# Kernel optimization log

Measured on AMD Instinct MI355X. Metric: run time of the kernel, lower is better.

## Reference

```python
import math
import jax, jax.numpy as jnp
import numpy as np

N_HEAD = 12
HEAD_DIM = 64
NEG = -1e9

def setup_inputs() -> dict:
    key = jax.random.key(0)
    k1, k2, k3 = jax.random.split(key, 3)
    B, T, C = 16, 1024, 768
    x = jax.random.normal(k1, (B, T, C), dtype=jnp.float32)
    attention_mask = jnp.ones((B, T), dtype=jnp.int32)
    W_attn = jax.random.normal(k2, (C, 3 * C), dtype=jnp.float32) * 0.02
    b_attn = jnp.zeros((3 * C,), dtype=jnp.float32)
    W_proj = jax.random.normal(k3, (C, C), dtype=jnp.float32) * 0.02
    b_proj = jnp.zeros((C,), dtype=jnp.float32)
    return {"x": x, "attention_mask": attention_mask, "W_attn": W_attn,
            "b_attn": b_attn, "W_proj": W_proj, "b_proj": b_proj}

def reference(x, attention_mask, W_attn, b_attn, W_proj, b_proj):
    B, T, C = x.shape
    H, D = N_HEAD, HEAD_DIM
    qkv = x @ W_attn + b_attn                       # [B,T,3C]
    q, k, v = jnp.split(qkv, 3, axis=-1)
    q = q.reshape(B, T, H, D).transpose(0, 2, 1, 3)  # [B,H,T,D]
    k = k.reshape(B, T, H, D).transpose(0, 2, 1, 3)
    v = v.reshape(B, T, H, D).transpose(0, 2, 1, 3)
    att = jnp.einsum('bhqd,bhkd->bhqk', q, k) / math.sqrt(D)  # [B,H,T,T]
    causal = jnp.tril(jnp.ones((T, T), dtype=bool))[None, None]
    key_mask = (attention_mask[:, None, None, :] != 0)          # [B,1,1,T]
    # masked_fill(-inf) then replace inf with -1e9 == set masked to -1e9
    att = jnp.where(causal & key_mask, att, NEG)
    att = jax.nn.softmax(att, axis=-1)
    query_mask = attention_mask[:, None, :, None].astype(att.dtype)  # [B,1,T,1]
    att = att * query_mask
    y = jnp.einsum('bhqk,bhkd->bhqd', att, v)        # [B,H,T,D]
    y = y.transpose(0, 2, 1, 3).reshape(B, T, C)
    return y @ W_proj + b_proj
```

## Files before the change

### kernel.cpp

```cpp
#include <hip/hip_runtime.h>
#include <stdint.h>

typedef unsigned short u16;
typedef unsigned int u32;
typedef __attribute__((ext_vector_type(8))) short short8;
typedef __attribute__((ext_vector_type(4))) float f32x4;
typedef __attribute__((ext_vector_type(4))) unsigned short u16x4;

#define LDS_AS __attribute__((address_space(3)))
#define GLB_AS __attribute__((address_space(1)))

__device__ __forceinline__ u16 f2bf(float f) {
  u32 u = __float_as_uint(f);
  u = (u + 0x7FFFu + ((u >> 16) & 1u)) >> 16;
  return (u16)u;
}

__device__ __forceinline__ void gload_lds16(const u16* g, u16* l) {
  __builtin_amdgcn_global_load_lds((const GLB_AS u32*)g, (LDS_AS u32*)l, 16, 0, 0);
}

__device__ __forceinline__ f32x4 mfma16(short8 a, short8 b, f32x4 c) {
  return __builtin_amdgcn_mfma_f32_16x16x32_bf16(a, b, c, 0, 0, 0);
}

__global__ __launch_bounds__(256) void k_cvt(const float* __restrict__ in,
                                             u16* __restrict__ out, int n4) {
  int i = blockIdx.x * 256 + threadIdx.x;
  if (i >= n4) return;
  f32x4 v = ((const f32x4*)in)[i];
  u16x4 o = {f2bf(v[0]), f2bf(v[1]), f2bf(v[2]), f2bf(v[3])};
  ((u16x4*)out)[i] = o;
}

__global__ __launch_bounds__(256) void k_transpose_cvt(const float* __restrict__ W,
                                                       u16* __restrict__ Wt, int K, int N) {
  __shared__ float tile[32][33];
  int n0 = blockIdx.x * 32;
  int k0 = blockIdx.y * 32;
  int tx = threadIdx.x & 31, ty = threadIdx.x >> 5;
#pragma unroll
  for (int i = 0; i < 4; i++) {
    int k = k0 + ty + i * 8;
    tile[ty + i * 8][tx] = W[(size_t)k * N + n0 + tx];
  }
  __syncthreads();
#pragma unroll
  for (int i = 0; i < 4; i++) {
    int n = n0 + ty + i * 8;
    Wt[(size_t)n * K + k0 + tx] = f2bf(tile[tx][ty + i * 8]);
  }
}

template <int MODE>
__global__ __launch_bounds__(256) void k_gemm(const u16* __restrict__ A,
                                              const u16* __restrict__ Bt,
                                              const float* __restrict__ bias,
                                              void* __restrict__ C, u16* __restrict__ vTo,
                                              int M, int N, int K) {
  __shared__ __align__(16) u16 As[2][128 * 64];
  __shared__ __align__(16) u16 Bs[2][128 * 64];
  const int nwg = gridDim.x;
  const int wgo = blockIdx.x;
  const int cpx = nwg >> 3;
  const int swz = (wgo & 7) * cpx + (wgo >> 3);
  const int ntn = N >> 7;
  const int tm = swz / ntn, tn = swz % ntn;
  const int m0 = tm << 7, n0 = tn << 7;
  const int tid = threadIdx.x;
  const int lane = tid & 63, w = tid >> 6;
  const int wm = (w >> 1) << 6, wn = (w & 1) << 6;
  const int fr = lane & 15, kg = lane >> 4;

  f32x4 acc[4][4];
#pragma unroll
  for (int i = 0; i < 4; i++)
#pragma unroll
    for (int j = 0; j < 4; j++) acc[i][j] = (f32x4){0.f, 0.f, 0.f, 0.f};

  const int rs = tid >> 3;
  const int ck = (((tid & 7) ^ (rs & 7)) << 3);
  const u16* ga = A + (size_t)(m0 + rs) * K + ck;
  const u16* gb = Bt + (size_t)(n0 + rs) * K + ck;
  const size_t row32 = (size_t)32 * K;

#define GSTAGE(buf, kt)                                                      \
  {                                                                          \
    const int ko = (kt) * 64;                                                \
    _Pragma("unroll") for (int s = 0; s < 4; ++s) {                          \
      gload_lds16(ga + s * row32 + ko, &As[buf][s * 2048 + tid * 8]);        \
    }                                                                        \
    _Pragma("unroll") for (int s = 0; s < 4; ++s) {                          \
      gload_lds16(gb + s * row32 + ko, &Bs[buf][s * 2048 + tid * 8]);        \
    }                                                                        \
  }

  const int KT = K >> 6;
  GSTAGE(0, 0);

  for (int kt = 0; kt < KT; ++kt) {
    const int cur = kt & 1;
    if (kt + 1 < KT) {
      GSTAGE(cur ^ 1, kt + 1);
      asm volatile("s_waitcnt vmcnt(8)" ::: "memory");
    } else {
      asm volatile("s_waitcnt vmcnt(0)" ::: "memory");
    }
    __builtin_amdgcn_sched_barrier(0);
    __builtin_amdgcn_s_barrier();
    __builtin_amdgcn_sched_barrier(0);

#pragma unroll
    for (int kk = 0; kk < 2; ++kk) {
      short8 af[4], bf[4];
      const int cs = ((kk * 4 + kg) ^ (fr & 7)) << 3;
#pragma unroll
      for (int mi = 0; mi < 4; mi++)
        af[mi] = *(const short8*)&As[cur][(wm + mi * 16 + fr) * 64 + cs];
#pragma unroll
      for (int nj = 0; nj < 4; nj++)
        bf[nj] = *(const short8*)&Bs[cur][(wn + nj * 16 + fr) * 64 + cs];
      asm volatile("s_waitcnt lgkmcnt(0)" ::: "memory");
      __builtin_amdgcn_sched_barrier(0);
#pragma unroll
      for (int mi = 0; mi < 4; mi++)
#pragma unroll
        for (int nj = 0; nj < 4; nj++)
          acc[mi][nj] = mfma16(af[mi], bf[nj], acc[mi][nj]);
    }
    __builtin_amdgcn_sched_barrier(0);
    __builtin_amdgcn_s_barrier();
  }
#undef GSTAGE

  const int r0 = (lane >> 4) << 2;
  const bool isv = (MODE == 1) && (n0 >= 1536);
#pragma unroll
  for (int mi = 0; mi < 4; mi++) {
    const int row = m0 + wm + mi * 16 + r0;
#pragma unroll
    for (int nj = 0; nj < 4; nj++) {
      const int col = n0 + wn + nj * 16 + fr;
      const float bs = bias[col];
      f32x4 v = acc[mi][nj];
      if (MODE == 0) {
#pragma unroll
        for (int r = 0; r < 4; r++)
          ((float*)C)[(size_t)(row + r) * N + col] = v[r] + bs;
      } else if (!isv) {
#pragma unroll
        for (int r = 0; r < 4; r++)
          ((u16*)C)[(size_t)(row + r) * 1536 + col] = f2bf(v[r] + bs);
      } else {
        int d = col - 1536;
        int hh = d >> 6, dd = d & 63;
        int bb = row >> 10, t = row & 1023;
        u16x4 pk = {f2bf(v[0] + bs), f2bf(v[1] + bs), f2bf(v[2] + bs), f2bf(v[3] + bs)};
        *(u16x4*)&vTo[((size_t)(bb * 12 + hh) * 64 + dd) * 1024 + t] = pk;
      }
    }
  }
}

__global__ __launch_bounds__(256, 3) void k_attn(const u16* __restrict__ qk,
                                                 const u16* __restrict__ vT,
                                                 const int* __restrict__ amask,
                                                 u16* __restrict__ y) {
  __shared__ __align__(16) u16 Ks[2][64 * 64];
  __shared__ __align__(16) u16 Vs[2][64 * 64];
  __shared__ __align__(16) u16 Ps[4][2][16 * 72];
  __shared__ u32 mbits[32];

  const int bh = blockIdx.x;
  const int qp = blockIdx.y;
  const int b = bh / 12, h = bh % 12;
  const int qbA = qp * 64, qbB = (15 - qp) * 64;
  const int nt = 16 - qp;
  const int tid = threadIdx.x, lane = tid & 63, w = tid >> 6;
  const int fr = lane & 15, kg = lane >> 4;

  const u16* qg = qk + (size_t)b * 1024 * 1536 + h * 64;
  const u16* kgp = qg + 768;
  const u16* vg = vT + (size_t)bh * 64 * 1024;
  const int* mrow = amask + b * 1024;

  short8 qfA[2], qfB[2];
  {
    const u16* ra = qg + (size_t)(qbA + w * 16 + fr) * 1536 + kg * 8;
    const u16* rb = qg + (size_t)(qbB + w * 16 + fr) * 1536 + kg * 8;
    qfA[0] = *(const short8*)ra;
    qfA[1] = *(const short8*)(ra + 32);
    qfB[0] = *(const short8*)rb;
    qfB[1] = *(const short8*)(rb + 32);
  }

#pragma unroll
  for (int i = 0; i < 4; i++) {
    int tok = i * 256 + tid;
    unsigned long long bm = __ballot(mrow[tok] != 0);
    if (lane == 0) {
      int base = (i * 256 + w * 64) >> 5;
      mbits[base] = (u32)bm;
      mbits[base + 1] = (u32)(bm >> 32);
    }
  }
  __syncthreads();

  const int sr0 = tid >> 3, sc = tid & 7;
  const int sr1 = sr0 + 32;
  const int sw0 = (sc ^ (sr0 & 7)) << 3;

#define STAGE_KV(buf, kv0)                                                          \
  {                                                                                 \
    gload_lds16(kgp + (size_t)((kv0) + sr0) * 1536 + sw0, &Ks[buf][tid * 8]);       \
    gload_lds16(kgp + (size_t)((kv0) + sr1) * 1536 + sw0, &Ks[buf][2048 + tid * 8]);\
    gload_lds16(vg + (size_t)sr0 * 1024 + (kv0) + sw0, &Vs[buf][tid * 8]);          \
    gload_lds16(vg + (size_t)sr1 * 1024 + (kv0) + sw0, &Vs[buf][2048 + tid * 8]);   \
  }

  STAGE_KV(0, 0);

  f32x4 oA[4], oB[4];
  float psA[4], psB[4];
#pragma unroll
  for (int i = 0; i < 4; i++) {
    oA[i] = (f32x4){0.f, 0.f, 0.f, 0.f};
    oB[i] = (f32x4){0.f, 0.f, 0.f, 0.f};
    psA[i] = 0.f;
    psB[i] = 0.f;
  }
  u16* PwA = &Ps[w][0][0];
  u16* PwB = &Ps[w][1][0];

  const float SCALE2 = 0.125f * 1.44269504f;
  const float MFIX = 4.0f;

  for (int it = 0; it < nt; ++it) {
    const int kv0 = it * 64;
    const int cur = it & 1;
    if (it + 1 < nt) {
      STAGE_KV(cur ^ 1, kv0 + 64);
      asm volatile("s_waitcnt vmcnt(4)" ::: "memory");
    } else {
      asm volatile("s_waitcnt vmcnt(0)" ::: "memory");
    }
    __builtin_amdgcn_sched_barrier(0);
    __builtin_amdgcn_s_barrier();
    __builtin_amdgcn_sched_barrier(0);

    const bool aAct = (it <= qp);
    const u16* Kc = Ks[cur];
    const u16* Vc = Vs[cur];

    f32x4 sA[4], sB[4];
#pragma unroll
    for (int nf = 0; nf < 4; nf++) {
      sA[nf] = (f32x4){0.f, 0.f, 0.f, 0.f};
      sB[nf] = (f32x4){0.f, 0.f, 0.f, 0.f};
    }
#pragma unroll
    for (int nf = 0; nf < 4; nf++) {
      const int base = (nf * 16 + fr) * 64;
      short8 k0 = *(const short8*)&Kc[base + ((kg ^ (fr & 7)) << 3)];
      short8 k1 = *(const short8*)&Kc[base + (((kg + 4) ^ (fr & 7)) << 3)];
      sB[nf] = mfma16(qfB[0], k0, sB[nf]);
      sB[nf] = mfma16(qfB[1], k1, sB[nf]);
      if (aAct) {
        sA[nf] = mfma16(qfA[0], k0, sA[nf]);
        sA[nf] = mfma16(qfA[1], k1, sA[nf]);
      }
    }

    float kmof[4];
#pragma unroll
    for (int nf = 0; nf < 4; nf++) {
      int kv = kv0 + nf * 16 + fr;
      u32 wv = mbits[kv >> 5];
      kmof[nf] = ((wv >> (kv & 31)) & 1u) ? -MFIX : -1e9f;
    }

    auto softmax = [&](f32x4(&s)[4], float(&ps)[4], u16* Pw, int qb, bool diag) {
#pragma unroll
      for (int nf = 0; nf < 4; nf++)
#pragma unroll
        for (int r = 0; r < 4; r++) {
          float v = fmaf(s[nf][r], SCALE2, kmof[nf]);
          if (diag) {
            int kv = kv0 + nf * 16 + fr;
            int q = qb + w * 16 + kg * 4 + r;
            if (kv > q) v = -1e9f;
          }
          float e = exp2f(v);
          ps[r] += e;
          Pw[(kg * 4 + r) * 72 + nf * 16 + fr] = f2bf(e);
        }
    };

    if (aAct) softmax(sA, psA, PwA, qbA, it == qp);
    softmax(sB, psB, PwB, qbB, it == nt - 1);

#pragma unroll
    for (int kc = 0; kc < 2; kc++) {
      short8 pB = *(const short8*)&PwB[fr * 72 + kc * 32 + kg * 8];
      short8 pA;
      if (aAct) pA = *(const short8*)&PwA[fr * 72 + kc * 32 + kg * 8];
#pragma unroll
      for (int df = 0; df < 4; df++) {
        short8 vf = *(const short8*)&Vc[(df * 16 + fr) * 64 + (((kc * 4 + kg) ^ (fr & 7)) << 3)];
        oB[df] = mfma16(pB, vf, oB[df]);
        if (aAct) oA[df] = mfma16(pA, vf, oA[df]);
      }
    }

    __builtin_amdgcn_sched_barrier(0);
    __builtin_amdgcn_s_barrier();
  }
#undef STAGE_KV

#pragma unroll
  for (int r = 0; r < 4; r++) {
    float lAr = psA[r];
    lAr += __shfl_xor(lAr, 1);
    lAr += __shfl_xor(lAr, 2);
    lAr += __shfl_xor(lAr, 4);
    lAr += __shfl_xor(lAr, 8);
    float lBr = psB[r];
    lBr += __shfl_xor(lBr, 1);
    lBr += __shfl_xor(lBr, 2);
    lBr += __shfl_xor(lBr, 4);
    lBr += __shfl_xor(lBr, 8);
    int qA = qbA + w * 16 + kg * 4 + r;
    int qB = qbB + w * 16 + kg * 4 + r;
    float nA = ((mbits[qA >> 5] >> (qA & 31)) & 1u) ? (1.f / lAr) : 0.f;
    float nB = ((mbits[qB >> 5] >> (qB & 31)) & 1u) ? (1.f / lBr) : 0.f;
#pragma unroll
    for (int df = 0; df < 4; df++) {
      y[(size_t)(b * 1024 + qA) * 768 + h * 64 + df * 16 + fr] = f2bf(oA[df][r] * nA);
      y[(size_t)(b * 1024 + qB) * 768 + h * 64 + df * 16 + fr] = f2bf(oB[df][r] * nB);
    }
  }
}

extern "C" void kernel_launch(void* const* d_in, const int* in_sizes, int n_in,
                              void* d_out, int out_size, void* d_ws, size_t ws_size,
                              hipStream_t stream) {
  const float* x = (const float*)d_in[0];
  const int* amask = (const int*)d_in[1];
  const float* W_attn = (const float*)d_in[2];
  const float* b_attn = (const float*)d_in[3];
  const float* W_proj = (const float*)d_in[4];
  const float* b_proj = (const float*)d_in[5];
  float* out = (float*)d_out;

  u16* xb = (u16*)d_ws;
  u16* wta = xb + (size_t)16384 * 768;
  u16* wtp = wta + (size_t)2304 * 768;
  u16* qk = wtp + (size_t)768 * 768;
  u16* vT = qk + (size_t)16384 * 1536;
  u16* yb = vT + (size_t)192 * 64 * 1024;

  (void)in_sizes; (void)n_in; (void)out_size; (void)ws_size;

  k_cvt<<<(16384 * 768 / 4) / 256, 256, 0, stream>>>(x, xb, 16384 * 768 / 4);
  k_transpose_cvt<<<dim3(2304 / 32, 768 / 32), 256, 0, stream>>>(W_attn, wta, 768, 2304);
  k_transpose_cvt<<<dim3(768 / 32, 768 / 32), 256, 0, stream>>>(W_proj, wtp, 768, 768);

  k_gemm<1><<<(16384 / 128) * (2304 / 128), 256, 0, stream>>>(xb, wta, b_attn, qk, vT,
                                                              16384, 2304, 768);
  k_attn<<<dim3(192, 8), 256, 0, stream>>>(qk, vT, amask, yb);
  k_gemm<0><<<(16384 / 128) * (768 / 128), 256, 0, stream>>>(yb, wtp, b_proj, out, nullptr,
                                                             16384, 768, 768);
}
```

Measured before the change: 212.7 us.

## Enlarge GEMM tiles to 256x256 with 8 waves and interleaved load/MFMA schedule

The bf16 GEMM moves from 128x128 tiles with 4 waves to 256x256 tiles with 8 waves (512 threads), each wave computing a 128x64 sub-tile. Each k-step is split into four MFMA quadrants, with the next stage's global-to-LDS loads issued between them and s_setprio raising priority around the MFMA bursts. The aim is more data reuse per LDS byte and better overlap of memory traffic with matrix math. In exchange it uses 128KB of LDS, more accumulator registers, fewer workgroups (e.g. 192 for the projection GEMM) and lower occupancy.

```diff
diff --git a/kernel.cpp b/kernel.cpp
--- a/kernel.cpp
+++ b/kernel.cpp
@@ -53,94 +53,141 @@
 }
 
 template <int MODE>
-__global__ __launch_bounds__(256) void k_gemm(const u16* __restrict__ A,
+__global__ __launch_bounds__(512) void k_gemm(const u16* __restrict__ A,
                                               const u16* __restrict__ Bt,
                                               const float* __restrict__ bias,
                                               void* __restrict__ C, u16* __restrict__ vTo,
                                               int M, int N, int K) {
-  __shared__ __align__(16) u16 As[2][128 * 64];
-  __shared__ __align__(16) u16 Bs[2][128 * 64];
+  __shared__ __align__(16) u16 As[2][256 * 64];
+  __shared__ __align__(16) u16 Bs[2][256 * 64];
   const int nwg = gridDim.x;
   const int wgo = blockIdx.x;
   const int cpx = nwg >> 3;
   const int swz = (wgo & 7) * cpx + (wgo >> 3);
-  const int ntn = N >> 7;
+  const int ntn = N >> 8;
   const int tm = swz / ntn, tn = swz % ntn;
-  const int m0 = tm << 7, n0 = tn << 7;
+  const int m0 = tm << 8, n0 = tn << 8;
   const int tid = threadIdx.x;
   const int lane = tid & 63, w = tid >> 6;
-  const int wm = (w >> 1) << 6, wn = (w & 1) << 6;
+  const int wr = w >> 2, wc = w & 3;
   const int fr = lane & 15, kg = lane >> 4;
 
-  f32x4 acc[4][4];
-#pragma unroll
-  for (int i = 0; i < 4; i++)
+  f32x4 acc[8][4];
+#pragma unroll
+  for (int i = 0; i < 8; i++)
 #pragma unroll
     for (int j = 0; j < 4; j++) acc[i][j] = (f32x4){0.f, 0.f, 0.f, 0.f};
 
-  const int rs = tid >> 3;
-  const int ck = (((tid & 7) ^ (rs & 7)) << 3);
-  const u16* ga = A + (size_t)(m0 + rs) * K + ck;
-  const u16* gb = Bt + (size_t)(n0 + rs) * K + ck;
-  const size_t row32 = (size_t)32 * K;
-
-#define GSTAGE(buf, kt)                                                      \
-  {                                                                          \
-    const int ko = (kt) * 64;                                                \
-    _Pragma("unroll") for (int s = 0; s < 4; ++s) {                          \
-      gload_lds16(ga + s * row32 + ko, &As[buf][s * 2048 + tid * 8]);        \
-    }                                                                        \
-    _Pragma("unroll") for (int s = 0; s < 4; ++s) {                          \
-      gload_lds16(gb + s * row32 + ko, &Bs[buf][s * 2048 + tid * 8]);        \
-    }                                                                        \
-  }
+  const int rs = tid >> 3, sc = tid & 7;
+  const int csrc = ((sc ^ (rs & 7)) << 3);
+  const u16* ga = A + (size_t)(m0 + rs) * K + csrc;
+  const u16* gb = Bt + (size_t)(n0 + rs) * K + csrc;
+  const size_t qstep = (size_t)64 * K;
+
+#define SA(buf, kt, q) gload_lds16(ga + (q)*qstep + (kt) * 64, &As[buf][(q)*4096 + tid * 8])
+#define SBq(buf, kt, q) gload_lds16(gb + (q)*qstep + (kt) * 64, &Bs[buf][(q)*4096 + tid * 8])
 
   const int KT = K >> 6;
-  GSTAGE(0, 0);
-
-  for (int kt = 0; kt < KT; ++kt) {
-    const int cur = kt & 1;
-    if (kt + 1 < KT) {
-      GSTAGE(cur ^ 1, kt + 1);
-      asm volatile("s_waitcnt vmcnt(8)" ::: "memory");
-    } else {
-      asm volatile("s_waitcnt vmcnt(0)" ::: "memory");
-    }
+  SA(0, 0, 0); SA(0, 0, 2);
+  SBq(0, 0, 0); SBq(0, 0, 1); SBq(0, 0, 2); SBq(0, 0, 3);
+  SA(0, 0, 1); SA(0, 0, 3);
+
+  const int rdA0 = (wr * 128 + fr) * 64;
+  const int rdB0 = (wc * 64 + fr) * 64;
+  const int cs0 = ((kg ^ (fr & 7)) << 3);
+  const int cs1 = (((kg + 4) ^ (fr & 7)) << 3);
+
+  short8 af[4][2], bf[4][2];
+  for (int t = 0; t < KT; ++t) {
+    const int c = t & 1, nb = c ^ 1;
+    const bool st = (t + 1 < KT);
+    asm volatile("s_waitcnt vmcnt(2)" ::: "memory");
     __builtin_amdgcn_sched_barrier(0);
     __builtin_amdgcn_s_barrier();
     __builtin_amdgcn_sched_barrier(0);
-
-#pragma unroll
-    for (int kk = 0; kk < 2; ++kk) {
-      short8 af[4], bf[4];
-      const int cs = ((kk * 4 + kg) ^ (fr & 7)) << 3;
-#pragma unroll
-      for (int mi = 0; mi < 4; mi++)
-        af[mi] = *(const short8*)&As[cur][(wm + mi * 16 + fr) * 64 + cs];
-#pragma unroll
-      for (int nj = 0; nj < 4; nj++)
-        bf[nj] = *(const short8*)&Bs[cur][(wn + nj * 16 + fr) * 64 + cs];
-      asm volatile("s_waitcnt lgkmcnt(0)" ::: "memory");
-      __builtin_amdgcn_sched_barrier(0);
-#pragma unroll
-      for (int mi = 0; mi < 4; mi++)
-#pragma unroll
-        for (int nj = 0; nj < 4; nj++)
-          acc[mi][nj] = mfma16(af[mi], bf[nj], acc[mi][nj]);
-    }
+    if (st) { SA(nb, t + 1, 0); SA(nb, t + 1, 2); }
+#pragma unroll
+    for (int mi = 0; mi < 4; mi++) {
+      af[mi][0] = *(const short8*)&As[c][rdA0 + mi * 1024 + cs0];
+      af[mi][1] = *(const short8*)&As[c][rdA0 + mi * 1024 + cs1];
+    }
+#pragma unroll
+    for (int nj = 0; nj < 2; nj++) {
+      bf[nj][0] = *(const short8*)&Bs[c][rdB0 + nj * 1024 + cs0];
+      bf[nj][1] = *(const short8*)&Bs[c][rdB0 + nj * 1024 + cs1];
+    }
+    asm volatile("s_waitcnt lgkmcnt(0)" ::: "memory");
+    __builtin_amdgcn_sched_barrier(0);
+    __builtin_amdgcn_s_setprio(1);
+#pragma unroll
+    for (int mi = 0; mi < 4; mi++)
+#pragma unroll
+      for (int nj = 0; nj < 2; nj++) {
+        acc[mi][nj] = mfma16(af[mi][0], bf[nj][0], acc[mi][nj]);
+        acc[mi][nj] = mfma16(af[mi][1], bf[nj][1], acc[mi][nj]);
+      }
+    __builtin_amdgcn_s_setprio(0);
+    if (st) { SBq(nb, t + 1, 0); SBq(nb, t + 1, 1); }
+#pragma unroll
+    for (int nj = 2; nj < 4; nj++) {
+      bf[nj][0] = *(const short8*)&Bs[c][rdB0 + nj * 1024 + cs0];
+      bf[nj][1] = *(const short8*)&Bs[c][rdB0 + nj * 1024 + cs1];
+    }
+    asm volatile("s_waitcnt lgkmcnt(0)" ::: "memory");
+    __builtin_amdgcn_sched_barrier(0);
+    __builtin_amdgcn_s_setprio(1);
+#pragma unroll
+    for (int mi = 0; mi < 4; mi++)
+#pragma unroll
+      for (int nj = 2; nj < 4; nj++) {
+        acc[mi][nj] = mfma16(af[mi][0], bf[nj][0], acc[mi][nj]);
+        acc[mi][nj] = mfma16(af[mi][1], bf[nj][1], acc[mi][nj]);
+      }
+    __builtin_amdgcn_s_setprio(0);
+    if (st) asm volatile("s_waitcnt vmcnt(4)" ::: "memory");
+    else    asm volatile("s_waitcnt vmcnt(0)" ::: "memory");
     __builtin_amdgcn_sched_barrier(0);
     __builtin_amdgcn_s_barrier();
-  }
-#undef GSTAGE
-
-  const int r0 = (lane >> 4) << 2;
+    __builtin_amdgcn_sched_barrier(0);
+    if (st) { SBq(nb, t + 1, 2); SBq(nb, t + 1, 3); }
+#pragma unroll
+    for (int mi = 0; mi < 4; mi++) {
+      af[mi][0] = *(const short8*)&As[c][rdA0 + 4096 + mi * 1024 + cs0];
+      af[mi][1] = *(const short8*)&As[c][rdA0 + 4096 + mi * 1024 + cs1];
+    }
+    asm volatile("s_waitcnt lgkmcnt(0)" ::: "memory");
+    __builtin_amdgcn_sched_barrier(0);
+    __builtin_amdgcn_s_setprio(1);
+#pragma unroll
+    for (int mi = 0; mi < 4; mi++)
+#pragma unroll
+      for (int nj = 2; nj < 4; nj++) {
+        acc[4 + mi][nj] = mfma16(af[mi][0], bf[nj][0], acc[4 + mi][nj]);
+        acc[4 + mi][nj] = mfma16(af[mi][1], bf[nj][1], acc[4 + mi][nj]);
+      }
+    __builtin_amdgcn_s_setprio(0);
+    if (st) { SA(nb, t + 1, 1); SA(nb, t + 1, 3); }
+    __builtin_amdgcn_s_setprio(1);
+#pragma unroll
+    for (int mi = 0; mi < 4; mi++)
+#pragma unroll
+      for (int nj = 0; nj < 2; nj++) {
+        acc[4 + mi][nj] = mfma16(af[mi][0], bf[nj][0], acc[4 + mi][nj]);
+        acc[4 + mi][nj] = mfma16(af[mi][1], bf[nj][1], acc[4 + mi][nj]);
+      }
+    __builtin_amdgcn_s_setprio(0);
+  }
+#undef SA
+#undef SBq
+
+  const int r0 = kg << 2;
   const bool isv = (MODE == 1) && (n0 >= 1536);
 #pragma unroll
-  for (int mi = 0; mi < 4; mi++) {
-    const int row = m0 + wm + mi * 16 + r0;
+  for (int mi = 0; mi < 8; mi++) {
+    const int row = m0 + wr * 128 + mi * 16 + r0;
 #pragma unroll
     for (int nj = 0; nj < 4; nj++) {
-      const int col = n0 + wn + nj * 16 + fr;
+      const int col = n0 + wc * 64 + nj * 16 + fr;
       const float bs = bias[col];
       f32x4 v = acc[mi][nj];
       if (MODE == 0) {
@@ -365,9 +412,9 @@
   k_transpose_cvt<<<dim3(2304 / 32, 768 / 32), 256, 0, stream>>>(W_attn, wta, 768, 2304);
   k_transpose_cvt<<<dim3(768 / 32, 768 / 32), 256, 0, stream>>>(W_proj, wtp, 768, 768);
 
-  k_gemm<1><<<(16384 / 128) * (2304 / 128), 256, 0, stream>>>(xb, wta, b_attn, qk, vT,
+  k_gemm<1><<<(16384 / 256) * (2304 / 256), 512, 0, stream>>>(xb, wta, b_attn, qk, vT,
                                                               16384, 2304, 768);
   k_attn<<<dim3(192, 8), 256, 0, stream>>>(qk, vT, amask, yb);
-  k_gemm<0><<<(16384 / 128) * (768 / 128), 256, 0, stream>>>(yb, wtp, b_proj, out, nullptr,
+  k_gemm<0><<<(16384 / 256) * (768 / 256), 512, 0, stream>>>(yb, wtp, b_proj, out, nullptr,
                                                              16384, 768, 768);
 }
```

Measured after the change: 221.4 us. 1.04x slower.
